# Performance work log

Hardware: AMD Instinct MI355X
Metric: run time of the kernel (lower is better)

## Reference

```python
import jax, jax.numpy as jnp
import numpy as np

H = 8192  # hidden_dimension
D = 8192  # trailing feature width of x


def setup_inputs() -> dict:
    key = jax.random.key(0)
    k_x, k_w = jax.random.split(key)
    x = jax.random.normal(k_x, (H, D), dtype=jnp.float32)
    # torch.nn.init.uniform_(weights, 0, 0.9); bias initialized to 0
    weights = jax.random.uniform(k_w, (H - 1, 1), dtype=jnp.float32, minval=0.0, maxval=0.9)
    bias = jnp.zeros((H - 1, 1), dtype=jnp.float32)
    return {"x": x, "weights": weights, "bias": bias}


def reference(x, weights, bias):
    # Original: for 5 generations, y[i] = x[i] + x[i-1]*w[i-1] + b[i-1] (i>0),
    # reading from the ORIGINAL x each time -> idempotent, single affine op.
    # weights/bias are [H-1, 1] and broadcast over the trailing D axis.
    shifted = x[1:] + x[:-1] * weights + bias  # [H-1, D]
    y = jnp.concatenate([x[:1], shifted], axis=0)  # [H, D]
    return y
```

## Files before the change

kernel.cpp:

```cpp
#include <hip/hip_runtime.h>


#define H_DIM 8192
#define D_DIM 8192
#define D4 (D_DIM / 4)
#define N4 (H_DIM * D4)
#define BLOCK 256

typedef float v4f __attribute__((ext_vector_type(4)));

__global__ __launch_bounds__(BLOCK, 8) void lateral_kernel(
    const v4f* __restrict__ x,
    const float* __restrict__ w,
    const float* __restrict__ b,
    v4f* __restrict__ y) {

    const int idx = blockIdx.x * BLOCK + threadIdx.x;

    v4f cur = x[idx];
    v4f o;
    if (idx >= D4) {
        const int row = idx >> 11;
        v4f pv = x[idx - D4];
        const float wi = w[row - 1];
        const float bi = b[row - 1];
        o.x = fmaf(pv.x, wi, cur.x + bi);
        o.y = fmaf(pv.y, wi, cur.y + bi);
        o.z = fmaf(pv.z, wi, cur.z + bi);
        o.w = fmaf(pv.w, wi, cur.w + bi);
    } else {
        o = cur;
    }
    __builtin_nontemporal_store(o, &y[idx]);
}

extern "C" void kernel_launch(void* const* d_in, const int* in_sizes, int n_in,
                              void* d_out, int out_size, void* d_ws, size_t ws_size,
                              hipStream_t stream) {
    const v4f*   x = (const v4f*)d_in[0];
    const float* w = (const float*)d_in[1];
    const float* b = (const float*)d_in[2];
    v4f* y = (v4f*)d_out;

    lateral_kernel<<<N4 / BLOCK, BLOCK, 0, stream>>>(x, w, b, y);
}
```

Measured before the change: 422.7 us.

## Process eight rows per thread to reuse previous-row loads in registers

Measured after the change: 429.4 us. No clear change (+1.6%).

```diff
diff --git a/kernel.cpp b/kernel.cpp
--- a/kernel.cpp
+++ b/kernel.cpp
@@ -4,34 +4,57 @@
 #define H_DIM 8192
 #define D_DIM 8192
 #define D4 (D_DIM / 4)
-#define N4 (H_DIM * D4)
+#define ROWS 8
 #define BLOCK 256
 
 typedef float v4f __attribute__((ext_vector_type(4)));
 
-__global__ __launch_bounds__(BLOCK, 8) void lateral_kernel(
+__global__ __launch_bounds__(BLOCK, 4) void lateral_kernel(
     const v4f* __restrict__ x,
     const float* __restrict__ w,
     const float* __restrict__ b,
     v4f* __restrict__ y) {
 
-    const int idx = blockIdx.x * BLOCK + threadIdx.x;
+    const int r0   = blockIdx.y * ROWS;
+    const int c    = blockIdx.x * BLOCK + threadIdx.x;
+    const int base = r0 * D4 + c;
 
-    v4f cur = x[idx];
-    v4f o;
-    if (idx >= D4) {
-        const int row = idx >> 11;
-        v4f pv = x[idx - D4];
-        const float wi = w[row - 1];
-        const float bi = b[row - 1];
-        o.x = fmaf(pv.x, wi, cur.x + bi);
-        o.y = fmaf(pv.y, wi, cur.y + bi);
-        o.z = fmaf(pv.z, wi, cur.z + bi);
-        o.w = fmaf(pv.w, wi, cur.w + bi);
-    } else {
-        o = cur;
+    v4f xs[ROWS];
+    #pragma unroll
+    for (int j = 0; j < ROWS; ++j)
+        xs[j] = x[base + j * D4];
+
+    v4f prev = {0.f, 0.f, 0.f, 0.f};
+    if (r0 > 0)
+        prev = x[base - D4];
+
+    float wr[ROWS], br[ROWS];
+    #pragma unroll
+    for (int j = 0; j < ROWS; ++j) {
+        const int row = r0 + j;
+        wr[j] = (row > 0) ? w[row - 1] : 0.f;
+        br[j] = (row > 0) ? b[row - 1] : 0.f;
     }
-    __builtin_nontemporal_store(o, &y[idx]);
+
+    v4f o[ROWS];
+    v4f p = prev;
+    #pragma unroll
+    for (int j = 0; j < ROWS; ++j) {
+        const v4f cur = xs[j];
+        v4f oo;
+        oo.x = fmaf(p.x, wr[j], cur.x + br[j]);
+        oo.y = fmaf(p.y, wr[j], cur.y + br[j]);
+        oo.z = fmaf(p.z, wr[j], cur.z + br[j]);
+        oo.w = fmaf(p.w, wr[j], cur.w + br[j]);
+        o[j] = oo;
+        p = cur;
+    }
+    if (r0 == 0)
+        o[0] = xs[0];
+
+    #pragma unroll
+    for (int j = 0; j < ROWS; ++j)
+        __builtin_nontemporal_store(o[j], &y[base + j * D4]);
 }
 
 extern "C" void kernel_launch(void* const* d_in, const int* in_sizes, int n_in,
@@ -42,5 +65,6 @@
     const float* b = (const float*)d_in[2];
     v4f* y = (v4f*)d_out;
 
-    lateral_kernel<<<N4 / BLOCK, BLOCK, 0, stream>>>(x, w, b, y);
+    dim3 grid(D4 / BLOCK, H_DIM / ROWS);
+    lateral_kernel<<<grid, BLOCK, 0, stream>>>(x, w, b, y);
 }
```
